# Optimization experiments

Hardware: AMD Instinct MI355X
Metric: run time of the kernel (lower is better)

The kernel has to match this reference:

```python
import jax, jax.numpy as jnp
import numpy as np

B, Q, A, D, H = 64, 16, 4096, 128, 8
HD = D // H
FF = 512

def _layernorm(x, g, b, eps=1e-5):
    mu = jnp.mean(x, axis=-1, keepdims=True)
    var = jnp.var(x, axis=-1, keepdims=True)
    return (x - mu) * jax.lax.rsqrt(var + eps) * g + b

def setup_inputs() -> dict:
    key = jax.random.key(0)
    ks = jax.random.split(key, 8)
    s = 0.05  # weight scale for sane numerics
    return {
        'q': jax.random.normal(ks[0], (B, Q, D), jnp.float32),
        'embed': jax.random.normal(ks[1], (B, A, D), jnp.float32),
        'attn_mask': jnp.zeros((B, Q, A), jnp.bool_),
        'batch_mask': jax.random.randint(ks[2], (B,), 0, B, jnp.int32),
        'W_kv': jax.random.normal(ks[3], (2 * D, D), jnp.float32) * s,
        'W_q': jax.random.normal(ks[4], (D, D), jnp.float32) * s,
        'W_o': jax.random.normal(ks[5], (D, D), jnp.float32) * s,
        'ln1_g': jnp.ones((D,), jnp.float32),
        'ln1_b': jnp.zeros((D,), jnp.float32),
        'ln2_g': jnp.ones((D,), jnp.float32),
        'ln2_b': jnp.zeros((D,), jnp.float32),
        'alpha1': jnp.full((1,), 0.1, jnp.float32),
        'alpha2': jnp.full((1,), 0.1, jnp.float32),
        'w_ff': jax.random.normal(ks[6], (2 * FF, D), jnp.float32) * s,
        'b_ff': jnp.zeros((2 * FF,), jnp.float32),
        'w_ff_out': jax.random.normal(ks[7], (D, FF), jnp.float32) * s,
        'b_ff_out': jnp.zeros((D,), jnp.float32),
    }

def reference(q, embed, attn_mask, batch_mask, W_kv, W_q, W_o,
              ln1_g, ln1_b, ln2_g, ln2_b, alpha1, alpha2,
              w_ff, b_ff, w_ff_out, b_ff_out):
    # cache_keys: project city embeddings to K/V, split into heads
    kv = embed @ W_kv.T                      # [B, A, 2D]
    k, v = jnp.split(kv, 2, axis=-1)
    k = k.reshape(B, A, H, HD).transpose(0, 2, 1, 3)   # [B, H, A, HD]
    v = v.reshape(B, A, H, HD).transpose(0, 2, 1, 3)   # [B, H, A, HD]

    # pre-norm query projection
    q_norm = _layernorm(q, ln1_g, ln1_b)
    gq = (q_norm @ W_q.T).reshape(B, Q, H, HD).transpose(0, 2, 1, 3)  # [B, H, Q, HD]

    # batch gather on cached K/V
    k = k[batch_mask]
    v = v[batch_mask]

    score = jnp.einsum('bhqd,bhkd->bhqk', gq, k) / jnp.sqrt(jnp.float32(HD))
    score = jnp.where(attn_mask[:, None, :, :], -jnp.inf, score)
    attn = jax.nn.softmax(score, axis=-1)
    ctx = jnp.einsum('bhqk,bhkd->bhqd', attn, v)        # [B, H, Q, HD]
    ctx = ctx.transpose(0, 2, 1, 3).reshape(B, Q, D)
    att_out = ctx @ W_o.T

    hidden = q + alpha1 * att_out
    hn = _layernorm(hidden, ln2_g, ln2_b)
    ab = hn @ w_ff.T + b_ff                              # [B, Q, 2*FF]
    a, b = jnp.split(ab, 2, axis=-1)
    h = jax.nn.silu(a) * b
    ff_out = h @ w_ff_out.T + b_ff_out
    return hidden + alpha2 * ff_out
```

## Files before the change

kernel.cpp:

```cpp
#include <hip/hip_runtime.h>
#include <cstdint>
#include <cstddef>

#define B_ 64
#define Q_ 16
#define A_ 4096
#define D_ 128
#define H_ 8
#define HD_ 16
#define FF_ 512
#define GQ_SCALE 0.36067376022224085f

typedef __attribute__((ext_vector_type(4))) float f32x4;
typedef __attribute__((ext_vector_type(8))) __bf16 bf16x8;
typedef __attribute__((ext_vector_type(4))) short s16x4;

static __device__ __forceinline__ short f2bf(float f) {
    __bf16 h = (__bf16)f;
    return __builtin_bit_cast(short, h);
}

static __device__ __forceinline__ f32x4 mfma32(bf16x8 a, bf16x8 b, f32x4 c) {
    return __builtin_amdgcn_mfma_f32_16x16x32_bf16(a, b, c, 0, 0, 0);
}

__global__ __launch_bounds__(256) void kprep(
    const float* __restrict__ wkv, const float* __restrict__ wo,
    const float* __restrict__ wff, const float* __restrict__ wffo,
    short* __restrict__ o_kv, short* __restrict__ o_wo,
    short* __restrict__ o_ff, short* __restrict__ o_ffo)
{
    int i = (blockIdx.x * 256 + threadIdx.x) * 4;
    const float* src; short* dst; int off;
    if (i < 32768)       { src = wkv;  dst = o_kv;  off = i; }
    else if (i < 49152)  { src = wo;   dst = o_wo;  off = i - 32768; }
    else if (i < 180224) { src = wff;  dst = o_ff;  off = i - 49152; }
    else                 { src = wffo; dst = o_ffo; off = i - 180224; }
    float4 v = *(const float4*)(src + off);
    s16x4 p;
    p[0] = f2bf(v.x); p[1] = f2bf(v.y); p[2] = f2bf(v.z); p[3] = f2bf(v.w);
    *(s16x4*)(dst + off) = p;
}

__global__ __launch_bounds__(128) void kgq(
    const float* __restrict__ qin, const float* __restrict__ g1,
    const float* __restrict__ b1, const float* __restrict__ Wq,
    short* __restrict__ gq)
{
    __shared__ float sx[128];
    __shared__ float red[2];
    int r = blockIdx.x;
    int t = threadIdx.x;
    float x = qin[(size_t)r * 128 + t];
    float v = x;
    for (int o = 32; o > 0; o >>= 1) v += __shfl_down(v, o);
    if ((t & 63) == 0) red[t >> 6] = v;
    __syncthreads();
    float mu = (red[0] + red[1]) * (1.f / 128.f);
    __syncthreads();
    float d = x - mu;
    v = d * d;
    for (int o = 32; o > 0; o >>= 1) v += __shfl_down(v, o);
    if ((t & 63) == 0) red[t >> 6] = v;
    __syncthreads();
    float var = (red[0] + red[1]) * (1.f / 128.f);
    float xn = d * rsqrtf(var + 1e-5f) * g1[t] + b1[t];
    sx[t] = xn;
    __syncthreads();
    float acc = 0.f;
    const float4* wr = (const float4*)(Wq + (size_t)t * 128);
    const float4* xv = (const float4*)sx;
    for (int i = 0; i < 32; ++i) {
        float4 a = wr[i], bb = xv[i];
        acc += a.x * bb.x + a.y * bb.y + a.z * bb.z + a.w * bb.w;
    }
    gq[(size_t)r * 128 + t] = f2bf(acc * GQ_SCALE);
}

__global__ __launch_bounds__(512, 4) void kattn(
    const float* __restrict__ embed, const int* __restrict__ bmask,
    const unsigned char* __restrict__ amask, const short* __restrict__ wkv16,
    const short* __restrict__ gq, float* __restrict__ pml,
    float* __restrict__ pctx)
{
    __shared__ __align__(16) short lds[36864];
    const int KR  = 8192;
    const int VR  = 16384;
    const int PR  = 24576;
    const int MK  = 32768;

    const int chunk = blockIdx.x;
    const int b     = blockIdx.y;
    const int t = threadIdx.x;
    const int w = t >> 6;
    const int l = t & 63;
    const int g = l >> 4;
    const int c = l & 15;
    const int s = bmask[b];
    const int a0 = chunk * 512;

    {
        unsigned char* mlb = (unsigned char*)&lds[MK];
        int qr = t >> 5, off = (t & 31) * 16;
        *(uint4*)&mlb[qr * 512 + off] =
            *(const uint4*)&amask[((size_t)(b * 16 + qr)) * 4096 + a0 + off];
    }

    const bool kw = (w < 4);
    const int wrow0 = kw ? (w * 32) : (128 + (w - 4) * 32);
    bf16x8 wf[2][4];
    for (int xf = 0; xf < 2; ++xf)
        for (int kf = 0; kf < 4; ++kf)
            wf[xf][kf] = *(const bf16x8*)(const void*)
                         (wkv16 + (size_t)(wrow0 + xf * 16 + c) * 128
                                + kf * 32 + g * 8);

    bf16x8 gqA;
    if (g < 2)
        gqA = *(const bf16x8*)(const void*)
              (gq + ((size_t)(b * 16 + c)) * 128 + w * 16 + g * 8);
    else { bf16x8 z = {}; gqA = z; }

    f32x4 ctx = {0.f, 0.f, 0.f, 0.f};
    float mrun[4], lrun[4];
    for (int r = 0; r < 4; ++r) { mrun[r] = -3.0e38f; lrun[r] = 0.f; }

    const float* esrc = embed + ((size_t)s * 4096 + a0) * 128;
    const int srow = t >> 5;
    const int scol = (t & 31) * 4;

    float4 pf[4];
    auto loadregs = [&](int ts) {
        for (int p = 0; p < 4; ++p)
            pf[p] = *(const float4*)(esrc + (size_t)(ts * 64 + srow + p * 16) * 128
                                     + scol);
    };
    loadregs(0);

    for (int ts = 0; ts < 8; ++ts) {
        __syncthreads();
        for (int p = 0; p < 4; ++p) {
            int rr = srow + p * 16;
            int byte = (rr * 256 + scol * 2) ^ ((rr & 7) << 4);
            s16x4 pk;
            pk[0] = f2bf(pf[p].x); pk[1] = f2bf(pf[p].y);
            pk[2] = f2bf(pf[p].z); pk[3] = f2bf(pf[p].w);
            *(s16x4*)(void*)((char*)lds + byte) = pk;
        }
        if (ts < 7) loadregs(ts + 1);
        __syncthreads();
        for (int kb4 = 0; kb4 < 4; ++kb4) {
            bf16x8 eb[4];
            for (int kf = 0; kf < 4; ++kf) {
                int rr = kb4 * 16 + c;
                int byte = (rr * 256 + kf * 64 + g * 16) ^ ((rr & 7) << 4);
                eb[kf] = *(const bf16x8*)(const void*)((char*)lds + byte);
            }
            for (int xf = 0; xf < 2; ++xf) {
                f32x4 acc = {0.f, 0.f, 0.f, 0.f};
                if (kw) { for (int kf = 0; kf < 4; ++kf) acc = mfma32(wf[xf][kf], eb[kf], acc); }
                else    { for (int kf = 0; kf < 4; ++kf) acc = mfma32(eb[kf], wf[xf][kf], acc); }
                s16x4 pk;
                pk[0] = f2bf(acc[0]); pk[1] = f2bf(acc[1]);
                pk[2] = f2bf(acc[2]); pk[3] = f2bf(acc[3]);
                if (kw) {
                    int h = 2 * w + xf;
                    int e = (h * 4 + kb4) * 256 + (g >> 1) * 128 + c * 8 + (g & 1) * 4;
                    *(s16x4*)(void*)&lds[KR + e] = pk;
                } else {
                    int h = 2 * (w - 4) + xf;
                    int e = (h * 2 + (kb4 >> 1)) * 512
                          + ((2 * (kb4 & 1) + (g >> 1)) * 16 + c) * 8 + (g & 1) * 4;
                    *(s16x4*)(void*)&lds[VR + e] = pk;
                }
            }
        }
        __syncthreads();
        float mb[4][4];
        {
            const unsigned char* mlb = (const unsigned char*)&lds[MK];
            for (int kb = 0; kb < 4; ++kb)
                for (int r = 0; r < 4; ++r)
                    mb[kb][r] = mlb[(4 * g + r) * 512 + ts * 64 + kb * 16 + c]
                                ? -1.0e30f : 0.0f;
        }
        f32x4 sc[4];
        for (int kb = 0; kb < 4; ++kb) {
            bf16x8 kB = *(const bf16x8*)(const void*)
                        &lds[KR + (w * 4 + kb) * 256 + (g * 16 + c) * 8];
            f32x4 z = {0.f, 0.f, 0.f, 0.f};
            sc[kb] = mfma32(gqA, kB, z);
        }
        float al[4], rs[4];
        for (int r = 0; r < 4; ++r) {
            float s0 = sc[0][r] + mb[0][r], s1 = sc[1][r] + mb[1][r];
            float s2 = sc[2][r] + mb[2][r], s3 = sc[3][r] + mb[3][r];
            sc[0][r] = s0; sc[1][r] = s1; sc[2][r] = s2; sc[3][r] = s3;
            float tm = fmaxf(fmaxf(s0, s1), fmaxf(s2, s3));
            for (int o = 1; o < 16; o <<= 1) tm = fmaxf(tm, __shfl_xor(tm, o));
            float mn = fmaxf(mrun[r], tm);
            al[r] = exp2f(mrun[r] - mn);
            mrun[r] = mn;
        }
        for (int r = 0; r < 4; ++r) {
            float p0 = exp2f(sc[0][r] - mrun[r]);
            float p1 = exp2f(sc[1][r] - mrun[r]);
            float p2 = exp2f(sc[2][r] - mrun[r]);
            float p3 = exp2f(sc[3][r] - mrun[r]);
            sc[0][r] = p0; sc[1][r] = p1; sc[2][r] = p2; sc[3][r] = p3;
            float qsum = p0 + p1 + p2 + p3;
            for (int o = 1; o < 16; o <<= 1) qsum += __shfl_xor(qsum, o);
            rs[r] = qsum;
        }
        for (int r = 0; r < 4; ++r) {
            lrun[r] = lrun[r] * al[r] + rs[r];
            ctx[r] *= al[r];
        }
        for (int kb = 0; kb < 4; ++kb) {
            int base = PR + w * 1024 + (kb >> 1) * 512;
            int khi = 2 * (kb & 1) + (c >> 3);
            for (int r = 0; r < 4; ++r)
                lds[base + (khi * 16 + 4 * g + r) * 8 + (c & 7)] = f2bf(sc[kb][r]);
        }
        for (int k2 = 0; k2 < 2; ++k2) {
            bf16x8 pA = *(const bf16x8*)(const void*)
                        &lds[PR + w * 1024 + k2 * 512 + (g * 16 + c) * 8];
            bf16x8 vB = *(const bf16x8*)(const void*)
                        &lds[VR + (w * 2 + k2) * 512 + (g * 16 + c) * 8];
            ctx = mfma32(pA, vB, ctx);
        }
    }
    size_t base = (((size_t)b * 8 + w) * 8 + chunk) * 16;
    for (int r = 0; r < 4; ++r)
        pctx[(base + 4 * g + r) * 16 + c] = ctx[r];
    if (c == 0) {
        for (int r = 0; r < 4; ++r) {
            pml[(base + 4 * g + r) * 2 + 0] = mrun[r];
            pml[(base + 4 * g + r) * 2 + 1] = lrun[r];
        }
    }
}

__global__ __launch_bounds__(256, 2) void ktail(
    const float* __restrict__ pml, const float* __restrict__ pctx,
    const short* __restrict__ wo16, const float* __restrict__ qin,
    const float* __restrict__ alpha1, const float* __restrict__ g2,
    const float* __restrict__ b2, const short* __restrict__ wff16,
    const float* __restrict__ bff, const short* __restrict__ wffo16,
    const float* __restrict__ bffo, const float* __restrict__ alpha2,
    float* __restrict__ out)
{
    __shared__ __align__(16) short sctx[2048];
    __shared__ __align__(16) float shid[2048];
    __shared__ __align__(16) short shn[2048];
    __shared__ __align__(16) short shm[8192];
    const int b = blockIdx.x;
    const int t = threadIdx.x;
    const int w = t >> 6, l = t & 63, g = l >> 4, c = l & 15;
    (void)l;

    {
        int hq = t >> 1, vh = t & 1;
        int h = hq >> 4, qq = hq & 15;
        const float* pm = pml + (((size_t)b * 8 + h) * 8) * 32 + qq * 2;
        float M = -3.0e38f;
        for (int cc = 0; cc < 8; ++cc) M = fmaxf(M, pm[cc * 32]);
        float L = 0.f;
        float cx[8] = {0.f,0.f,0.f,0.f,0.f,0.f,0.f,0.f};
        for (int cc = 0; cc < 8; ++cc) {
            float f = exp2f(pm[cc * 32] - M);
            L += pm[cc * 32 + 1] * f;
            const float* pc = pctx + ((((size_t)b * 8 + h) * 8 + cc) * 16 + qq) * 16
                            + vh * 8;
            for (int j = 0; j < 8; ++j) cx[j] += pc[j] * f;
        }
        float inv = 1.f / L;
        s16x4 p0, p1;
        for (int j = 0; j < 4; ++j) p0[j] = f2bf(cx[j] * inv);
        for (int j = 0; j < 4; ++j) p1[j] = f2bf(cx[4 + j] * inv);
        int off = (h * 2 + vh) * 128 + qq * 8;
        *(s16x4*)&sctx[off] = p0;
        *(s16x4*)&sctx[off + 4] = p1;
    }
    __syncthreads();
    {
        float a1 = alpha1[0];
        bf16x8 cA[4];
        for (int kf = 0; kf < 4; ++kf)
            cA[kf] = *(const bf16x8*)(const void*)&sctx[(kf * 4 + g) * 128 + c * 8];
        for (int nf = 0; nf < 2; ++nf) {
            int dcol = w * 32 + nf * 16 + c;
            f32x4 acc = {0.f, 0.f, 0.f, 0.f};
            for (int kf = 0; kf < 4; ++kf) {
                bf16x8 wB = *(const bf16x8*)(const void*)
                            (wo16 + (size_t)dcol * 128 + kf * 32 + g * 8);
                acc = mfma32(cA[kf], wB, acc);
            }
            for (int r = 0; r < 4; ++r) {
                int q = 4 * g + r;
                float hid = qin[((size_t)b * 16 + q) * 128 + dcol] + a1 * acc[r];
                shid[q * 128 + dcol] = hid;
            }
        }
    }
    __syncthreads();
    {
        int row = t >> 4, ln = t & 15;
        float x[8], sum = 0.f, sq = 0.f;
        for (int j = 0; j < 8; ++j) {
            x[j] = shid[row * 128 + ln * 8 + j];
            sum += x[j]; sq += x[j] * x[j];
        }
        for (int o = 1; o < 16; o <<= 1) {
            sum += __shfl_xor(sum, o);
            sq  += __shfl_xor(sq, o);
        }
        float mu = sum * (1.f / 128.f);
        float var = sq * (1.f / 128.f) - mu * mu;
        float rstd = rsqrtf(var + 1e-5f);
        s16x4 h0, h1;
        for (int j = 0; j < 4; ++j)
            h0[j] = f2bf((x[j] - mu) * rstd * g2[ln * 8 + j] + b2[ln * 8 + j]);
        for (int j = 0; j < 4; ++j)
            h1[j] = f2bf((x[4 + j] - mu) * rstd * g2[ln * 8 + 4 + j] + b2[ln * 8 + 4 + j]);
        int off = ln * 128 + row * 8;
        *(s16x4*)&shn[off] = h0;
        *(s16x4*)&shn[off + 4] = h1;
    }
    __syncthreads();
    {
        bf16x8 hA[4];
        for (int kf = 0; kf < 4; ++kf)
            hA[kf] = *(const bf16x8*)(const void*)&shn[(kf * 4 + g) * 128 + c * 8];
        for (int nf = 0; nf < 8; ++nf) {
            int arow = w * 128 + nf * 16 + c;
            int brow = 512 + arow;
            f32x4 aa = {0.f,0.f,0.f,0.f}, ab = {0.f,0.f,0.f,0.f};
            for (int kf = 0; kf < 4; ++kf) {
                bf16x8 wa = *(const bf16x8*)(const void*)
                            (wff16 + (size_t)arow * 128 + kf * 32 + g * 8);
                bf16x8 wb = *(const bf16x8*)(const void*)
                            (wff16 + (size_t)brow * 128 + kf * 32 + g * 8);
                aa = mfma32(hA[kf], wa, aa);
                ab = mfma32(hA[kf], wb, ab);
            }
            float ba = bff[arow], bb2 = bff[brow];
            for (int r = 0; r < 4; ++r) {
                float a = aa[r] + ba, bb = ab[r] + bb2;
                float hv = a * bb / (1.f + __expf(-a));
                shm[(arow >> 3) * 128 + (4 * g + r) * 8 + (c & 7)] = f2bf(hv);
            }
        }
    }
    __syncthreads();
    {
        float a2 = alpha2[0];
        for (int nf = 0; nf < 2; ++nf) {
            int dcol = w * 32 + nf * 16 + c;
            f32x4 acc = {0.f, 0.f, 0.f, 0.f};
            for (int kf = 0; kf < 16; ++kf) {
                bf16x8 hA = *(const bf16x8*)(const void*)
                            &shm[(kf * 4 + g) * 128 + c * 8];
                bf16x8 wB = *(const bf16x8*)(const void*)
                            (wffo16 + (size_t)dcol * 512 + kf * 32 + g * 8);
                acc = mfma32(hA, wB, acc);
            }
            float bo = bffo[dcol];
            for (int r = 0; r < 4; ++r) {
                int q = 4 * g + r;
                out[((size_t)b * 16 + q) * 128 + dcol] =
                    shid[q * 128 + dcol] + a2 * (acc[r] + bo);
            }
        }
    }
}

extern "C" void kernel_launch(void* const* d_in, const int* in_sizes, int n_in,
                              void* d_out, int out_size, void* d_ws, size_t ws_size,
                              hipStream_t stream)
{
    (void)in_sizes; (void)n_in; (void)out_size; (void)ws_size;
    const float* qin   = (const float*)d_in[0];
    const float* embed = (const float*)d_in[1];
    const unsigned char* amask = (const unsigned char*)d_in[2];
    const int*   bmask = (const int*)d_in[3];
    const float* Wkv   = (const float*)d_in[4];
    const float* Wq    = (const float*)d_in[5];
    const float* Wo    = (const float*)d_in[6];
    const float* g1    = (const float*)d_in[7];
    const float* b1    = (const float*)d_in[8];
    const float* g2    = (const float*)d_in[9];
    const float* b2    = (const float*)d_in[10];
    const float* al1   = (const float*)d_in[11];
    const float* al2   = (const float*)d_in[12];
    const float* wff   = (const float*)d_in[13];
    const float* bff   = (const float*)d_in[14];
    const float* wffo  = (const float*)d_in[15];
    const float* bffo  = (const float*)d_in[16];
    float* out = (float*)d_out;

    char* ws = (char*)d_ws;
    short* gqb    = (short*)(ws + 0);
    float* pml    = (float*)(ws + 262144);
    float* pctx   = (float*)(ws + 786432);
    short* wkv16  = (short*)(ws + 4980736);
    short* wo16   = (short*)(ws + 5046272);
    short* wff16  = (short*)(ws + 5079040);
    short* wffo16 = (short*)(ws + 5341184);

    kprep<<<dim3(240),   dim3(256), 0, stream>>>(Wkv, Wo, wff, wffo,
                                                 wkv16, wo16, wff16, wffo16);
    kgq  <<<dim3(1024),  dim3(128), 0, stream>>>(qin, g1, b1, Wq, gqb);
    kattn<<<dim3(8, 64), dim3(512), 0, stream>>>(embed, bmask, amask, wkv16,
                                                 gqb, pml, pctx);
    ktail<<<dim3(64),    dim3(256), 0, stream>>>(pml, pctx, wo16, qin, al1,
                                                 g2, b2, wff16, bff, wffo16,
                                                 bffo, al2, out);
}
```

Measured before the change: 271.8 us.

## Skip per-element mask decode when tile is unmasked; widen tail kernel to 512 threads

In the attention kernel, each wave first checks a packed 16-byte chunk of the boolean mask and, if no lane sees any masked entry, fills the bias with zeros instead of doing sixteen byte loads and selects per lane. Separately, the tail kernel doubles its block to 512 threads and splits each phase (partial-softmax merge, Wo projection, layernorm, FFN up and down) so every thread does half the previous work. This aims to cut LDS traffic in the attention loop and raise parallelism in the 64-block tail. The mask fast path keeps exact semantics, and it adds an extra LDS load plus a wave vote in every iteration.

```diff
diff --git a/kernel.cpp b/kernel.cpp
--- a/kernel.cpp
+++ b/kernel.cpp
@@ -176,13 +176,21 @@
             }
         }
         __syncthreads();
+        const unsigned char* mlb = (const unsigned char*)&lds[MK];
         float mb[4][4];
         {
-            const unsigned char* mlb = (const unsigned char*)&lds[MK];
-            for (int kb = 0; kb < 4; ++kb)
-                for (int r = 0; r < 4; ++r)
-                    mb[kb][r] = mlb[(4 * g + r) * 512 + ts * 64 + kb * 16 + c]
-                                ? -1.0e30f : 0.0f;
+            uint4 mchk = *(const uint4*)
+                         &mlb[(4 * g + (c & 3)) * 512 + ts * 64 + (c >> 2) * 16];
+            int any = (mchk.x | mchk.y | mchk.z | mchk.w) != 0;
+            if (__any(any)) {
+                for (int kb = 0; kb < 4; ++kb)
+                    for (int r = 0; r < 4; ++r)
+                        mb[kb][r] = mlb[(4 * g + r) * 512 + ts * 64 + kb * 16 + c]
+                                    ? -1.0e30f : 0.0f;
+            } else {
+                for (int kb = 0; kb < 4; ++kb)
+                    for (int r = 0; r < 4; ++r) mb[kb][r] = 0.0f;
+            }
         }
         f32x4 sc[4];
         for (int kb = 0; kb < 4; ++kb) {
@@ -241,7 +249,7 @@
     }
 }
 
-__global__ __launch_bounds__(256, 2) void ktail(
+__global__ __launch_bounds__(512, 2) void ktail(
     const float* __restrict__ pml, const float* __restrict__ pctx,
     const short* __restrict__ wo16, const float* __restrict__ qin,
     const float* __restrict__ alpha1, const float* __restrict__ g2,
@@ -260,27 +268,25 @@
     (void)l;
 
     {
-        int hq = t >> 1, vh = t & 1;
+        int hq = t >> 2, vh = t & 3;
         int h = hq >> 4, qq = hq & 15;
         const float* pm = pml + (((size_t)b * 8 + h) * 8) * 32 + qq * 2;
         float M = -3.0e38f;
         for (int cc = 0; cc < 8; ++cc) M = fmaxf(M, pm[cc * 32]);
         float L = 0.f;
-        float cx[8] = {0.f,0.f,0.f,0.f,0.f,0.f,0.f,0.f};
+        float cx[4] = {0.f, 0.f, 0.f, 0.f};
         for (int cc = 0; cc < 8; ++cc) {
             float f = exp2f(pm[cc * 32] - M);
             L += pm[cc * 32 + 1] * f;
             const float* pc = pctx + ((((size_t)b * 8 + h) * 8 + cc) * 16 + qq) * 16
-                            + vh * 8;
-            for (int j = 0; j < 8; ++j) cx[j] += pc[j] * f;
+                            + vh * 4;
+            for (int j = 0; j < 4; ++j) cx[j] += pc[j] * f;
         }
         float inv = 1.f / L;
-        s16x4 p0, p1;
-        for (int j = 0; j < 4; ++j) p0[j] = f2bf(cx[j] * inv);
-        for (int j = 0; j < 4; ++j) p1[j] = f2bf(cx[4 + j] * inv);
-        int off = (h * 2 + vh) * 128 + qq * 8;
-        *(s16x4*)&sctx[off] = p0;
-        *(s16x4*)&sctx[off + 4] = p1;
+        s16x4 p;
+        for (int j = 0; j < 4; ++j) p[j] = f2bf(cx[j] * inv);
+        int off = (h * 2 + (vh >> 1)) * 128 + qq * 8 + (vh & 1) * 4;
+        *(s16x4*)&sctx[off] = p;
     }
     __syncthreads();
     {
@@ -288,52 +294,47 @@
         bf16x8 cA[4];
         for (int kf = 0; kf < 4; ++kf)
             cA[kf] = *(const bf16x8*)(const void*)&sctx[(kf * 4 + g) * 128 + c * 8];
-        for (int nf = 0; nf < 2; ++nf) {
-            int dcol = w * 32 + nf * 16 + c;
-            f32x4 acc = {0.f, 0.f, 0.f, 0.f};
-            for (int kf = 0; kf < 4; ++kf) {
-                bf16x8 wB = *(const bf16x8*)(const void*)
-                            (wo16 + (size_t)dcol * 128 + kf * 32 + g * 8);
-                acc = mfma32(cA[kf], wB, acc);
-            }
-            for (int r = 0; r < 4; ++r) {
-                int q = 4 * g + r;
-                float hid = qin[((size_t)b * 16 + q) * 128 + dcol] + a1 * acc[r];
-                shid[q * 128 + dcol] = hid;
-            }
-        }
-    }
-    __syncthreads();
-    {
-        int row = t >> 4, ln = t & 15;
-        float x[8], sum = 0.f, sq = 0.f;
-        for (int j = 0; j < 8; ++j) {
-            x[j] = shid[row * 128 + ln * 8 + j];
+        int dcol = w * 16 + c;
+        f32x4 acc = {0.f, 0.f, 0.f, 0.f};
+        for (int kf = 0; kf < 4; ++kf) {
+            bf16x8 wB = *(const bf16x8*)(const void*)
+                        (wo16 + (size_t)dcol * 128 + kf * 32 + g * 8);
+            acc = mfma32(cA[kf], wB, acc);
+        }
+        for (int r = 0; r < 4; ++r) {
+            int q = 4 * g + r;
+            float hid = qin[((size_t)b * 16 + q) * 128 + dcol] + a1 * acc[r];
+            shid[q * 128 + dcol] = hid;
+        }
+    }
+    __syncthreads();
+    {
+        int row = t >> 5, ln = t & 31;
+        float x[4], sum = 0.f, sq = 0.f;
+        for (int j = 0; j < 4; ++j) {
+            x[j] = shid[row * 128 + ln * 4 + j];
             sum += x[j]; sq += x[j] * x[j];
         }
-        for (int o = 1; o < 16; o <<= 1) {
+        for (int o = 1; o < 32; o <<= 1) {
             sum += __shfl_xor(sum, o);
             sq  += __shfl_xor(sq, o);
         }
         float mu = sum * (1.f / 128.f);
         float var = sq * (1.f / 128.f) - mu * mu;
         float rstd = rsqrtf(var + 1e-5f);
-        s16x4 h0, h1;
+        s16x4 hh;
         for (int j = 0; j < 4; ++j)
-            h0[j] = f2bf((x[j] - mu) * rstd * g2[ln * 8 + j] + b2[ln * 8 + j]);
-        for (int j = 0; j < 4; ++j)
-            h1[j] = f2bf((x[4 + j] - mu) * rstd * g2[ln * 8 + 4 + j] + b2[ln * 8 + 4 + j]);
-        int off = ln * 128 + row * 8;
-        *(s16x4*)&shn[off] = h0;
-        *(s16x4*)&shn[off + 4] = h1;
+            hh[j] = f2bf((x[j] - mu) * rstd * g2[ln * 4 + j] + b2[ln * 4 + j]);
+        int off = (ln >> 1) * 128 + row * 8 + (ln & 1) * 4;
+        *(s16x4*)&shn[off] = hh;
     }
     __syncthreads();
     {
         bf16x8 hA[4];
         for (int kf = 0; kf < 4; ++kf)
             hA[kf] = *(const bf16x8*)(const void*)&shn[(kf * 4 + g) * 128 + c * 8];
-        for (int nf = 0; nf < 8; ++nf) {
-            int arow = w * 128 + nf * 16 + c;
+        for (int nf = 0; nf < 4; ++nf) {
+            int arow = w * 64 + nf * 16 + c;
             int brow = 512 + arow;
             f32x4 aa = {0.f,0.f,0.f,0.f}, ab = {0.f,0.f,0.f,0.f};
             for (int kf = 0; kf < 4; ++kf) {
@@ -355,22 +356,20 @@
     __syncthreads();
     {
         float a2 = alpha2[0];
-        for (int nf = 0; nf < 2; ++nf) {
-            int dcol = w * 32 + nf * 16 + c;
-            f32x4 acc = {0.f, 0.f, 0.f, 0.f};
-            for (int kf = 0; kf < 16; ++kf) {
-                bf16x8 hA = *(const bf16x8*)(const void*)
-                            &shm[(kf * 4 + g) * 128 + c * 8];
-                bf16x8 wB = *(const bf16x8*)(const void*)
-                            (wffo16 + (size_t)dcol * 512 + kf * 32 + g * 8);
-                acc = mfma32(hA, wB, acc);
-            }
-            float bo = bffo[dcol];
-            for (int r = 0; r < 4; ++r) {
-                int q = 4 * g + r;
-                out[((size_t)b * 16 + q) * 128 + dcol] =
-                    shid[q * 128 + dcol] + a2 * (acc[r] + bo);
-            }
+        int dcol = w * 16 + c;
+        f32x4 acc = {0.f, 0.f, 0.f, 0.f};
+        for (int kf = 0; kf < 16; ++kf) {
+            bf16x8 hA = *(const bf16x8*)(const void*)
+                        &shm[(kf * 4 + g) * 128 + c * 8];
+            bf16x8 wB = *(const bf16x8*)(const void*)
+                        (wffo16 + (size_t)dcol * 512 + kf * 32 + g * 8);
+            acc = mfma32(hA, wB, acc);
+        }
+        float bo = bffo[dcol];
+        for (int r = 0; r < 4; ++r) {
+            int q = 4 * g + r;
+            out[((size_t)b * 16 + q) * 128 + dcol] =
+                shid[q * 128 + dcol] + a2 * (acc[r] + bo);
         }
     }
 }
@@ -413,7 +412,7 @@
     kgq  <<<dim3(1024),  dim3(128), 0, stream>>>(qin, g1, b1, Wq, gqb);
     kattn<<<dim3(8, 64), dim3(512), 0, stream>>>(embed, bmask, amask, wkv16,
                                                  gqb, pml, pctx);
-    ktail<<<dim3(64),    dim3(256), 0, stream>>>(pml, pctx, wo16, qin, al1,
+    ktail<<<dim3(64),    dim3(512), 0, stream>>>(pml, pctx, wo16, qin, al1,
                                                  g2, b2, wff16, bff, wffo16,
                                                  bffo, al2, out);
 }
```

Result: no change. 271.7 us (-0.0%).
